# Performance work log

Hardware: AMD Instinct MI355X
Metric: run time of the kernel (lower is better)

Reference implementation:

```python
import jax, jax.numpy as jnp
import numpy as np

N_NODES = 100000
N_EDGES = 1600000
IN_CH = 128
OUT_CH = 64
HID = 2 * OUT_CH


def setup_inputs() -> dict:
    key = jax.random.key(0)
    ks = jax.random.split(key, 9)
    x = jax.random.normal(ks[0], (N_NODES, IN_CH), dtype=jnp.float32)
    edge_index = jax.random.randint(ks[1], (2, N_EDGES), 0, N_NODES, dtype=jnp.int64)
    s = 0.05
    W1 = jax.random.normal(ks[2], (IN_CH, HID), dtype=jnp.float32) * s
    b1 = jnp.zeros((HID,), dtype=jnp.float32)
    Wmu = jax.random.normal(ks[3], (HID, OUT_CH), dtype=jnp.float32) * s
    bmu = jnp.zeros((OUT_CH,), dtype=jnp.float32)
    Wls = jax.random.normal(ks[4], (HID, OUT_CH), dtype=jnp.float32) * s
    bls = jnp.zeros((OUT_CH,), dtype=jnp.float32)
    eps = jax.random.normal(ks[5], (N_NODES, OUT_CH), dtype=jnp.float32)
    return {"x": x, "edge_index": edge_index, "W1": W1, "b1": b1,
            "Wmu": Wmu, "bmu": bmu, "Wls": Wls, "bls": bls, "eps": eps}


def _gcn_conv(x, W, b, src, dst, dis):
    # PyG GCNConv: out = D^{-1/2}(A+I)D^{-1/2} X W + b, self-loops added.
    h = x @ W  # [N, F]
    norm = dis[src] * dis[dst]  # per-edge symmetric norm
    msg = h[src] * norm[:, None]  # [E, F] gathered + scaled messages
    agg = jax.ops.segment_sum(msg, dst, num_segments=x.shape[0])
    agg = agg + h * (dis * dis)[:, None]  # self-loop term
    return agg + b


def reference(x, edge_index, W1, b1, Wmu, bmu, Wls, bls, eps):
    src, dst = edge_index[0], edge_index[1]
    N = x.shape[0]
    # degree over A + I (aggregation at dst, +1 for self loop)
    deg = jax.ops.segment_sum(jnp.ones_like(dst, dtype=x.dtype), dst,
                              num_segments=N) + 1.0
    dis = jax.lax.rsqrt(deg)  # deg >= 1, safe
    h = _gcn_conv(x, W1, b1, src, dst, dis)
    mu = _gcn_conv(h, Wmu, bmu, src, dst, dis)
    logstd = _gcn_conv(h, Wls, bls, src, dst, dis)
    z = mu + eps * jnp.exp(logstd)  # reparametrization trick
    return (z, mu, logstd)
```

## Files before the change

kernel.cpp:

```cpp
#include <hip/hip_runtime.h>
#include <hip/hip_bf16.h>


typedef unsigned int u32;
typedef unsigned short u16;
typedef unsigned char u8;
typedef __bf16 bf16x8 __attribute__((ext_vector_type(8)));
typedef float f32x4 __attribute__((ext_vector_type(4)));
typedef int i32x4 __attribute__((ext_vector_type(4)));

#define NBKT 196
#define BSH 9

__device__ __forceinline__ u16 f2bf(float f) {
    union { float f; u32 u; } v; v.f = f;
    u32 u = v.u;
    u += 0x7fffu + ((u >> 16) & 1u);
    return (u16)(u >> 16);
}
__device__ __forceinline__ float bflo(u32 p) {
    union { u32 u; float f; } v; v.u = p << 16; return v.f;
}
__device__ __forceinline__ float bfhi(u32 p) {
    union { u32 u; float f; } v; v.u = p & 0xffff0000u; return v.f;
}

__global__ __launch_bounds__(256) void bcount(const int* __restrict__ dst,
                                              u32* __restrict__ bucketCnt, int E) {
    __shared__ u32 hist[NBKT];
    int t = threadIdx.x;
    for (int i = t; i < NBKT; i += 256) hist[i] = 0;
    __syncthreads();
    int base = (blockIdx.x * 256 + t) * 4;
    if (base + 3 < E) {
        i32x4 d4 = __builtin_nontemporal_load((const i32x4*)(dst + base));
        atomicAdd(&hist[d4.x >> BSH], 1u);
        atomicAdd(&hist[d4.y >> BSH], 1u);
        atomicAdd(&hist[d4.z >> BSH], 1u);
        atomicAdd(&hist[d4.w >> BSH], 1u);
    } else {
        for (int i = base; i < E; ++i) atomicAdd(&hist[dst[i] >> BSH], 1u);
    }
    __syncthreads();
    for (int i = t; i < NBKT; i += 256)
        if (hist[i]) atomicAdd(&bucketCnt[i], hist[i]);
}

__global__ __launch_bounds__(256) void bscan(const u32* __restrict__ bucketCnt,
                                             u32* __restrict__ bucketStart,
                                             u32* __restrict__ bucketCur,
                                             u32* __restrict__ rowstart,
                                             int N, int E) {
    __shared__ u32 s[256];
    int t = threadIdx.x;
    u32 v = (t < NBKT) ? bucketCnt[t] : 0u;
    s[t] = v;
    for (int off = 1; off < 256; off <<= 1) {
        __syncthreads();
        u32 add = (t >= off) ? s[t - off] : 0u;
        __syncthreads();
        s[t] += add;
    }
    __syncthreads();
    if (t < NBKT) {
        u32 ex = s[t] - v;
        bucketStart[t] = ex;
        bucketCur[t] = ex;
        if (t == NBKT - 1) bucketStart[NBKT] = s[t];
    }
    if (t == 0) rowstart[N] = (u32)(E + N);
}

__global__ __launch_bounds__(256) void bscatter(const int* __restrict__ src,
                                                const int* __restrict__ dst,
                                                u32* __restrict__ bucketCur,
                                                u32* __restrict__ bksrc,
                                                u32* __restrict__ bkdst, int E) {
    __shared__ u32 hist[NBKT], lstart[NBKT], gbase[NBKT];
    __shared__ u32 sA[256];
    __shared__ u32 stS[1024], stD[1024];
    int t = threadIdx.x;
    int e0 = blockIdx.x * 1024;
    int m = min(1024, E - e0);
    for (int i = t; i < NBKT; i += 256) hist[i] = 0;
    __syncthreads();

    int sv[4], dv[4]; u32 rk[4];
    int base = e0 + t * 4;
    bool vec = (base + 3 < E);
    if (vec) {
        i32x4 s4 = __builtin_nontemporal_load((const i32x4*)(src + base));
        i32x4 d4 = __builtin_nontemporal_load((const i32x4*)(dst + base));
        sv[0] = s4.x; sv[1] = s4.y; sv[2] = s4.z; sv[3] = s4.w;
        dv[0] = d4.x; dv[1] = d4.y; dv[2] = d4.z; dv[3] = d4.w;
#pragma unroll
        for (int j = 0; j < 4; ++j) rk[j] = atomicAdd(&hist[dv[j] >> BSH], 1u);
    } else {
#pragma unroll
        for (int j = 0; j < 4; ++j) {
            if (base + j < E) {
                sv[j] = src[base + j]; dv[j] = dst[base + j];
                rk[j] = atomicAdd(&hist[dv[j] >> BSH], 1u);
            }
        }
    }
    __syncthreads();
    sA[t] = (t < NBKT) ? hist[t] : 0u;
    for (int off = 1; off < 256; off <<= 1) {
        __syncthreads();
        u32 add = (t >= off) ? sA[t - off] : 0u;
        __syncthreads();
        sA[t] += add;
    }
    __syncthreads();
    if (t < NBKT) {
        lstart[t] = sA[t] - hist[t];
        if (hist[t]) gbase[t] = atomicAdd(&bucketCur[t], hist[t]);
    }
    __syncthreads();
#pragma unroll
    for (int j = 0; j < 4; ++j) {
        if (base + j < E) {
            int b = dv[j] >> BSH;
            u32 p = lstart[b] + rk[j];
            stS[p] = (u32)sv[j];
            stD[p] = (u32)dv[j];
        }
    }
    __syncthreads();
    for (int i = t; i < m; i += 256) {
        u32 d = stD[i];
        int b = (int)(d >> BSH);
        u32 g = gbase[b] + ((u32)i - lstart[b]);
        bksrc[g] = stS[i];
        bkdst[g] = d;
    }
}

__global__ __launch_bounds__(512) void bbuild(const u32* __restrict__ bksrc,
                                              const u32* __restrict__ bkdst,
                                              const u32* __restrict__ bucketStart,
                                              u32* __restrict__ rowstart,
                                              float* __restrict__ dis,
                                              int* __restrict__ csr, int N) {
    __shared__ u32 degL[512], exL[512];
    int t = threadIdx.x, b = blockIdx.x;
    int n0 = b << BSH;
    int nn = min(N - n0, 512);
    u32 ebeg = bucketStart[b], eend = bucketStart[b + 1];
    u32 cbase = ebeg + ((u32)b << BSH);
    degL[t] = 0;
    __syncthreads();
    for (u32 e = ebeg + t; e < eend; e += 512)
        atomicAdd(&degL[bkdst[e] - (u32)n0], 1u);
    __syncthreads();
    u32 v = degL[t] + ((t < nn) ? 1u : 0u);
    exL[t] = v;
    for (int off = 1; off < 512; off <<= 1) {
        __syncthreads();
        u32 add = (t >= off) ? exL[t - off] : 0u;
        __syncthreads();
        exL[t] += add;
    }
    __syncthreads();
    u32 rowbase = cbase + exL[t] - v;
    if (t < nn) {
        rowstart[n0 + t] = rowbase;
        dis[n0 + t] = rsqrtf((float)v);
        csr[rowbase] = n0 + t;
    }
    __syncthreads();
    exL[t] = rowbase + 1;
    __syncthreads();
    for (u32 e = ebeg + t; e < eend; e += 512) {
        u32 ln = bkdst[e] - (u32)n0;
        u32 pos = atomicAdd(&exL[ln], 1u);
        csr[pos] = (int)bksrc[e];
    }
}

__global__ __launch_bounds__(256) void fuse_w(const float* __restrict__ W1,
                                              const float* __restrict__ Wmu,
                                              const float* __restrict__ Wls,
                                              const float* __restrict__ b1,
                                              const float* __restrict__ bmu,
                                              const float* __restrict__ bls,
                                              u16* __restrict__ WfT,
                                              float* __restrict__ bb,
                                              float* __restrict__ bcat) {
    int idx = blockIdx.x * 256 + threadIdx.x;
    if (idx >= 16384) return;
    int k = idx >> 7, n = idx & 127;
    const float* Wcol = (n < 64) ? (Wmu + n) : (Wls + (n - 64));
    float acc = 0.f;
#pragma unroll 8
    for (int j = 0; j < 128; ++j) acc += W1[k * 128 + j] * Wcol[j * 64];
    WfT[n * 128 + k] = f2bf(acc);
    if (k == 0) {
        float accb = 0.f;
#pragma unroll 8
        for (int j = 0; j < 128; ++j) accb += b1[j] * Wcol[j * 64];
        bb[n] = accb;
        bcat[n] = (n < 64) ? bmu[n] : bls[n - 64];
    }
}

__global__ __launch_bounds__(256) void convert_x(const float* __restrict__ x,
                                                 const float* __restrict__ dis,
                                                 u32* __restrict__ xs,
                                                 u32* __restrict__ ts, int N) {
    long i = (long)blockIdx.x * 256 + threadIdx.x;
    long node = i >> 5;
    if (node > N) return;
    if (node == N) {
        ((uint2*)xs)[i] = make_uint2(0u, 0u);
        ((uint2*)ts)[i] = make_uint2(0u, 0u);
        return;
    }
    float dd = dis[node];
    f32x4 v = ((const f32x4*)x)[i];
    u32 p0 = (u32)f2bf(v[0] * dd) | ((u32)f2bf(v[1] * dd) << 16);
    u32 p1 = (u32)f2bf(v[2] * dd) | ((u32)f2bf(v[3] * dd) << 16);
    ((uint2*)xs)[i] = make_uint2(p0, p1);
}

__global__ __launch_bounds__(512) void g1gemm(const u32* __restrict__ xs,
                                              const int* __restrict__ csr,
                                              const u32* __restrict__ rowstart,
                                              const float* __restrict__ dis,
                                              const u16* __restrict__ WfT,
                                              const float* __restrict__ bb,
                                              u16* __restrict__ ts, int N,
                                              int nodeBase) {
    __shared__ __align__(16) u16 ytile[16][136];
    __shared__ float disS[16];
    int tid = threadIdx.x, blk = blockIdx.x;
    int wave = tid >> 6, lane = tid & 63;
    int nsub = lane >> 5;
    int h = (lane >> 4) & 1;
    int l = lane & 15;
    int nl = wave * 2 + nsub;
    int node = nodeBase + blk * 16 + nl;
    bool live = node < N;
    int nodeC = live ? node : 0;
    float dd = dis[nodeC];
    u32 beg = live ? rowstart[nodeC] : 0u;
    u32 end = live ? rowstart[nodeC + 1] : 0u;
    u32 cut = beg + ((end - beg + 1u) >> 1);
    u32 mybeg = h ? cut : beg;
    u32 myend = h ? end : cut;
    if (tid < 16)
        disS[tid] = (nodeBase + blk * 16 + tid < N) ? dis[nodeBase + blk * 16 + tid]
                                                    : 0.f;

    const uint4* xs4 = (const uint4*)xs;
    float a0 = 0.f, a1 = 0.f, a2 = 0.f, a3 = 0.f;
    float a4 = 0.f, a5 = 0.f, a6 = 0.f, a7 = 0.f;

    int sbase = nsub * 32 + h * 16;
    int s = (l < 8 && mybeg + (u32)l < myend) ? csr[mybeg + l] : N;
    for (u32 e0 = mybeg; e0 < myend; e0 += 8) {
        u32 e1 = e0 + 8;
        int sn = (l < 8 && e1 < myend && e1 + (u32)l < myend) ? csr[e1 + l] : N;
        uint4 w[8];
#pragma unroll
        for (int j = 0; j < 8; ++j) {
            int sj = __shfl(s, sbase + j);
            w[j] = xs4[(long)sj * 16 + l];
        }
#pragma unroll
        for (int j = 0; j < 8; ++j) {
            a0 += bflo(w[j].x); a1 += bfhi(w[j].x);
            a2 += bflo(w[j].y); a3 += bfhi(w[j].y);
            a4 += bflo(w[j].z); a5 += bfhi(w[j].z);
            a6 += bflo(w[j].w); a7 += bfhi(w[j].w);
        }
        s = sn;
    }
    a0 += __shfl_xor(a0, 16); a1 += __shfl_xor(a1, 16);
    a2 += __shfl_xor(a2, 16); a3 += __shfl_xor(a3, 16);
    a4 += __shfl_xor(a4, 16); a5 += __shfl_xor(a5, 16);
    a6 += __shfl_xor(a6, 16); a7 += __shfl_xor(a7, 16);

    uint4 o = make_uint4(0u, 0u, 0u, 0u);
    if (live) {
        o.x = (u32)f2bf(a0 * dd) | ((u32)f2bf(a1 * dd) << 16);
        o.y = (u32)f2bf(a2 * dd) | ((u32)f2bf(a3 * dd) << 16);
        o.z = (u32)f2bf(a4 * dd) | ((u32)f2bf(a5 * dd) << 16);
        o.w = (u32)f2bf(a6 * dd) | ((u32)f2bf(a7 * dd) << 16);
    }
    if (h == 0) *(uint4*)&ytile[nl][l * 8] = o;
    __syncthreads();

    int quad = lane >> 4, mn = l;
    bf16x8 af[4];
#pragma unroll
    for (int kk = 0; kk < 4; ++kk)
        af[kk] = *reinterpret_cast<const bf16x8*>(&ytile[mn][kk * 32 + quad * 8]);

    int col = wave * 16 + mn;
    f32x4 acc = {0.f, 0.f, 0.f, 0.f};
#pragma unroll
    for (int kk = 0; kk < 4; ++kk) {
        bf16x8 bf =
            *reinterpret_cast<const bf16x8*>(&WfT[col * 128 + kk * 32 + quad * 8]);
        acc = __builtin_amdgcn_mfma_f32_16x16x32_bf16(af[kk], bf, acc, 0, 0, 0);
    }
    float bc = bb[col];
#pragma unroll
    for (int r = 0; r < 4; ++r) {
        int row = quad * 4 + r;
        int gn = nodeBase + blk * 16 + row;
        if (gn < N)
            __builtin_nontemporal_store(f2bf((acc[r] + bc) * disS[row]),
                                        ts + (long)gn * 128 + col);
    }
}

__global__ __launch_bounds__(256) void gather2(const u32* __restrict__ ts,
                                               const int* __restrict__ csr,
                                               const u32* __restrict__ rowstart,
                                               const float* __restrict__ dis,
                                               const float* __restrict__ bcat,
                                               const float* __restrict__ eps,
                                               float* __restrict__ out, int N,
                                               int nodeBase) {
    int tid = threadIdx.x;
    int gw = (blockIdx.x * 256 + tid) >> 6;
    int lane = tid & 63;
    int nsub = lane >> 5, h = (lane >> 4) & 1, l = lane & 15;
    int node = nodeBase + gw * 2 + nsub;
    bool live = node < N;
    int nodeC = live ? node : 0;
    float dd = dis[nodeC];
    u32 beg = live ? rowstart[nodeC] : 0u;
    u32 end = live ? rowstart[nodeC + 1] : 0u;
    u32 cut = beg + ((end - beg + 1u) >> 1);
    u32 mybeg = h ? cut : beg;
    u32 myend = h ? end : cut;
    const uint4* ts4 = (const uint4*)ts;

    float a0 = 0.f, a1 = 0.f, a2 = 0.f, a3 = 0.f;
    float a4 = 0.f, a5 = 0.f, a6 = 0.f, a7 = 0.f;

    int sbase = nsub * 32 + h * 16;
    int s = (l < 8 && mybeg + (u32)l < myend) ? csr[mybeg + l] : N;
    for (u32 e0 = mybeg; e0 < myend; e0 += 8) {
        u32 e1 = e0 + 8;
        int sn = (l < 8 && e1 < myend && e1 + (u32)l < myend) ? csr[e1 + l] : N;
        uint4 w[8];
#pragma unroll
        for (int j = 0; j < 8; ++j) {
            int sj = __shfl(s, sbase + j);
            w[j] = ts4[(long)sj * 16 + l];
        }
#pragma unroll
        for (int j = 0; j < 8; ++j) {
            a0 += bflo(w[j].x); a1 += bfhi(w[j].x);
            a2 += bflo(w[j].y); a3 += bfhi(w[j].y);
            a4 += bflo(w[j].z); a5 += bfhi(w[j].z);
            a6 += bflo(w[j].w); a7 += bfhi(w[j].w);
        }
        s = sn;
    }
    a0 += __shfl_xor(a0, 16); a1 += __shfl_xor(a1, 16);
    a2 += __shfl_xor(a2, 16); a3 += __shfl_xor(a3, 16);
    a4 += __shfl_xor(a4, 16); a5 += __shfl_xor(a5, 16);
    a6 += __shfl_xor(a6, 16); a7 += __shfl_xor(a7, 16);

    int c0 = l * 8;
    f32x4 clo = ((const f32x4*)bcat)[2 * l], chi = ((const f32x4*)bcat)[2 * l + 1];
    float v0 = a0 * dd + clo[0];
    float v1 = a1 * dd + clo[1];
    float v2 = a2 * dd + clo[2];
    float v3 = a3 * dd + clo[3];
    float v4 = a4 * dd + chi[0];
    float v5 = a5 * dd + chi[1];
    float v6 = a6 * dd + chi[2];
    float v7 = a7 * dd + chi[3];

    int srcl = lane + 8;
    float w0 = __shfl(v0, srcl), w1 = __shfl(v1, srcl), w2 = __shfl(v2, srcl),
          w3 = __shfl(v3, srcl), w4 = __shfl(v4, srcl), w5 = __shfl(v5, srcl),
          w6 = __shfl(v6, srcl), w7 = __shfl(v7, srcl);

    if (!live || h != 0) return;
    long NO = (long)N * 64;
    if (l < 8) {
        float* mu = out + NO + (long)node * 64 + c0;
        __builtin_nontemporal_store(f32x4{v0, v1, v2, v3}, (f32x4*)mu);
        __builtin_nontemporal_store(f32x4{v4, v5, v6, v7}, (f32x4*)mu + 1);
        const f32x4* ep = (const f32x4*)(eps + (long)node * 64 + c0);
        f32x4 e0v = __builtin_nontemporal_load(ep);
        f32x4 e1v = __builtin_nontemporal_load(ep + 1);
        float* z = out + (long)node * 64 + c0;
        f32x4 z0 = {v0 + e0v[0] * __expf(w0), v1 + e0v[1] * __expf(w1),
                    v2 + e0v[2] * __expf(w2), v3 + e0v[3] * __expf(w3)};
        f32x4 z1 = {v4 + e1v[0] * __expf(w4), v5 + e1v[1] * __expf(w5),
                    v6 + e1v[2] * __expf(w6), v7 + e1v[3] * __expf(w7)};
        __builtin_nontemporal_store(z0, (f32x4*)z);
        __builtin_nontemporal_store(z1, (f32x4*)z + 1);
    } else {
        float* ls = out + 2 * NO + (long)node * 64 + (c0 - 64);
        __builtin_nontemporal_store(f32x4{v0, v1, v2, v3}, (f32x4*)ls);
        __builtin_nontemporal_store(f32x4{v4, v5, v6, v7}, (f32x4*)ls + 1);
    }
}

extern "C" void kernel_launch(void* const* d_in, const int* in_sizes, int n_in,
                              void* d_out, int out_size, void* d_ws, size_t ws_size,
                              hipStream_t stream) {
    const float* x   = (const float*)d_in[0];
    const int* ei    = (const int*)d_in[1];
    const float* W1  = (const float*)d_in[2];
    const float* b1  = (const float*)d_in[3];
    const float* Wmu = (const float*)d_in[4];
    const float* bmu = (const float*)d_in[5];
    const float* Wls = (const float*)d_in[6];
    const float* bls = (const float*)d_in[7];
    const float* eps = (const float*)d_in[8];
    float* out = (float*)d_out;

    const int N = in_sizes[0] / 128;
    const int E = in_sizes[1] / 2;
    const int* src = ei;
    const int* dst = ei + E;

    char* ws = (char*)d_ws;
    u32* rowstart    = (u32*)(ws + 0);
    u32* bucketCnt   = (u32*)(ws + 401408);
    u32* bucketStart = (u32*)(ws + 403456);
    u32* bucketCur   = (u32*)(ws + 405504);
    float* dis       = (float*)(ws + 407552);
    u16* WfT         = (u16*)(ws + 808960);
    float* bb        = (float*)(ws + 841728);
    float* bcat      = (float*)(ws + 842240);
    int* csr         = (int*)(ws + 843776);
    u32* xs          = (u32*)(ws + 7644160);
    u32* ts          = (u32*)(ws + 33244416);
    u32* bksrc       = (u32*)(ws + 33244416);
    u32* bkdst       = (u32*)(ws + 39644416);

    hipMemsetAsync(bucketCnt, 0, 1024, stream);

    int gridE4 = (E / 4 + 255) / 256;
    bcount<<<gridE4, 256, 0, stream>>>(dst, bucketCnt, E);
    bscan<<<1, 256, 0, stream>>>(bucketCnt, bucketStart, bucketCur, rowstart, N, E);
    bscatter<<<gridE4, 256, 0, stream>>>(src, dst, bucketCur, bksrc, bkdst, E);
    bbuild<<<NBKT, 512, 0, stream>>>(bksrc, bkdst, bucketStart, rowstart, dis,
                                     csr, N);

    fuse_w<<<64, 256, 0, stream>>>(W1, Wmu, Wls, b1, bmu, bls, WfT, bb, bcat);

    long Qc = (long)(N + 1) * 32;
    convert_x<<<(int)((Qc + 255) / 256), 256, 0, stream>>>(x, dis, xs, ts, N);

    int H = (N + 1) / 2;
    int gridT1 = (H + 15) / 16;
    int gridT2 = (N - H + 15) / 16;
    g1gemm<<<gridT1, 512, 0, stream>>>(xs, csr, rowstart, dis, WfT, bb,
                                       (u16*)ts, N, 0);
    g1gemm<<<gridT2, 512, 0, stream>>>(xs, csr, rowstart, dis, WfT, bb,
                                       (u16*)ts, N, H);

    int gridG1 = (H + 7) / 8;
    int gridG2 = (N - H + 7) / 8;
    gather2<<<gridG1, 256, 0, stream>>>(ts, csr, rowstart, dis, bcat, eps, out,
                                        N, 0);
    gather2<<<gridG2, 256, 0, stream>>>(ts, csr, rowstart, dis, bcat, eps, out,
                                        N, H);
}
```

Measured before the change: 408.5 us.

## Slice features into 16-channel planes so gathers work on cache-resident slices

```diff
diff --git a/kernel.cpp b/kernel.cpp
--- a/kernel.cpp
+++ b/kernel.cpp
@@ -8,6 +8,7 @@
 typedef __bf16 bf16x8 __attribute__((ext_vector_type(8)));
 typedef float f32x4 __attribute__((ext_vector_type(4)));
 typedef int i32x4 __attribute__((ext_vector_type(4)));
+typedef u32 u32x2 __attribute__((ext_vector_type(2)));
 
 #define NBKT 196
 #define BSH 9
@@ -68,7 +69,7 @@
         bucketCur[t] = ex;
         if (t == NBKT - 1) bucketStart[NBKT] = s[t];
     }
-    if (t == 0) rowstart[N] = (u32)(E + N);
+    if (t == 0) rowstart[N] = (u32)E;
 }
 
 __global__ __launch_bounds__(256) void bscatter(const int* __restrict__ src,
@@ -148,13 +149,12 @@
     int n0 = b << BSH;
     int nn = min(N - n0, 512);
     u32 ebeg = bucketStart[b], eend = bucketStart[b + 1];
-    u32 cbase = ebeg + ((u32)b << BSH);
     degL[t] = 0;
     __syncthreads();
     for (u32 e = ebeg + t; e < eend; e += 512)
         atomicAdd(&degL[bkdst[e] - (u32)n0], 1u);
     __syncthreads();
-    u32 v = degL[t] + ((t < nn) ? 1u : 0u);
+    u32 v = degL[t];
     exL[t] = v;
     for (int off = 1; off < 512; off <<= 1) {
         __syncthreads();
@@ -163,14 +163,13 @@
         exL[t] += add;
     }
     __syncthreads();
-    u32 rowbase = cbase + exL[t] - v;
+    u32 absbase = ebeg + exL[t] - v;
     if (t < nn) {
-        rowstart[n0 + t] = rowbase;
-        dis[n0 + t] = rsqrtf((float)v);
-        csr[rowbase] = n0 + t;
-    }
-    __syncthreads();
-    exL[t] = rowbase + 1;
+        rowstart[n0 + t] = absbase;
+        dis[n0 + t] = rsqrtf((float)v + 1.0f);
+    }
+    __syncthreads();
+    exL[t] = absbase;
     __syncthreads();
     for (u32 e = ebeg + t; e < eend; e += 512) {
         u32 ln = bkdst[e] - (u32)n0;
@@ -207,193 +206,198 @@
 
 __global__ __launch_bounds__(256) void convert_x(const float* __restrict__ x,
                                                  const float* __restrict__ dis,
-                                                 u32* __restrict__ xs,
-                                                 u32* __restrict__ ts, int N) {
+                                                 u32* __restrict__ xsP, int N) {
     long i = (long)blockIdx.x * 256 + threadIdx.x;
     long node = i >> 5;
+    int j = (int)(i & 31);
     if (node > N) return;
+    int s = j >> 2, q = j & 3;
+    u32x2* dst = (u32x2*)((char*)xsP + ((size_t)s * (N + 1) + node) * 32 + q * 8);
     if (node == N) {
-        ((uint2*)xs)[i] = make_uint2(0u, 0u);
-        ((uint2*)ts)[i] = make_uint2(0u, 0u);
+        u32x2 z = {0u, 0u};
+        *dst = z;
         return;
     }
     float dd = dis[node];
     f32x4 v = ((const f32x4*)x)[i];
-    u32 p0 = (u32)f2bf(v[0] * dd) | ((u32)f2bf(v[1] * dd) << 16);
-    u32 p1 = (u32)f2bf(v[2] * dd) | ((u32)f2bf(v[3] * dd) << 16);
-    ((uint2*)xs)[i] = make_uint2(p0, p1);
-}
-
-__global__ __launch_bounds__(512) void g1gemm(const u32* __restrict__ xs,
-                                              const int* __restrict__ csr,
-                                              const u32* __restrict__ rowstart,
-                                              const float* __restrict__ dis,
-                                              const u16* __restrict__ WfT,
-                                              const float* __restrict__ bb,
-                                              u16* __restrict__ ts, int N,
-                                              int nodeBase) {
+    u32x2 o;
+    o.x = (u32)f2bf(v[0] * dd) | ((u32)f2bf(v[1] * dd) << 16);
+    o.y = (u32)f2bf(v[2] * dd) | ((u32)f2bf(v[3] * dd) << 16);
+    *dst = o;
+}
+
+__global__ __launch_bounds__(256) void gather1s(const u32* __restrict__ xsP,
+                                                const int* __restrict__ csr,
+                                                const u32* __restrict__ rowstart,
+                                                const float* __restrict__ dis,
+                                                u32* __restrict__ ys, int N) {
+    int tid = threadIdx.x;
+    u32 bid = blockIdx.x;
+    int s = bid & 7;
+    int sg = tid >> 4, ll = tid & 15;
+    int j = ll >> 1, p = ll & 1;
+    int node = (int)(bid >> 3) * 16 + sg;
+    bool live = node < N;
+    int nodeC = live ? node : 0;
+    float dd = dis[nodeC];
+    u32 beg = rowstart[nodeC];
+    u32 end = live ? rowstart[nodeC + 1] : beg;
+    const uint4* base = (const uint4*)(xsP + (size_t)s * (N + 1) * 8);
+
+    float a0 = 0.f, a1 = 0.f, a2 = 0.f, a3 = 0.f;
+    float a4 = 0.f, a5 = 0.f, a6 = 0.f, a7 = 0.f;
+
+    u32 e0 = beg + (u32)j;
+    int idx = (e0 < end) ? csr[e0] : N;
+    for (u32 c = beg; c < end; c += 8) {
+        u32 c1 = c + 8;
+        int idxn = (c1 + (u32)j < end) ? csr[c1 + (u32)j] : N;
+        uint4 v = base[(size_t)idx * 2 + p];
+        a0 += bflo(v.x); a1 += bfhi(v.x);
+        a2 += bflo(v.y); a3 += bfhi(v.y);
+        a4 += bflo(v.z); a5 += bfhi(v.z);
+        a6 += bflo(v.w); a7 += bfhi(v.w);
+        idx = idxn;
+    }
+#pragma unroll
+    for (int m = 2; m <= 8; m <<= 1) {
+        a0 += __shfl_xor(a0, m); a1 += __shfl_xor(a1, m);
+        a2 += __shfl_xor(a2, m); a3 += __shfl_xor(a3, m);
+        a4 += __shfl_xor(a4, m); a5 += __shfl_xor(a5, m);
+        a6 += __shfl_xor(a6, m); a7 += __shfl_xor(a7, m);
+    }
+    if (j != 0) return;
+    uint4 sv = base[(size_t)nodeC * 2 + p];
+    a0 += bflo(sv.x); a1 += bfhi(sv.x);
+    a2 += bflo(sv.y); a3 += bfhi(sv.y);
+    a4 += bflo(sv.z); a5 += bfhi(sv.z);
+    a6 += bflo(sv.w); a7 += bfhi(sv.w);
+    if (!live) return;
+    uint4 o;
+    o.x = (u32)f2bf(a0 * dd) | ((u32)f2bf(a1 * dd) << 16);
+    o.y = (u32)f2bf(a2 * dd) | ((u32)f2bf(a3 * dd) << 16);
+    o.z = (u32)f2bf(a4 * dd) | ((u32)f2bf(a5 * dd) << 16);
+    o.w = (u32)f2bf(a6 * dd) | ((u32)f2bf(a7 * dd) << 16);
+    ((uint4*)ys)[((size_t)s * (N + 1) + node) * 2 + p] = o;
+}
+
+__global__ __launch_bounds__(256) void gemm1(const u32* __restrict__ ys,
+                                             const u16* __restrict__ WfT,
+                                             const float* __restrict__ bb,
+                                             const float* __restrict__ dis,
+                                             u16* __restrict__ tsP, int N) {
     __shared__ __align__(16) u16 ytile[16][136];
     __shared__ float disS[16];
     int tid = threadIdx.x, blk = blockIdx.x;
-    int wave = tid >> 6, lane = tid & 63;
-    int nsub = lane >> 5;
-    int h = (lane >> 4) & 1;
-    int l = lane & 15;
-    int nl = wave * 2 + nsub;
-    int node = nodeBase + blk * 16 + nl;
+    int node0 = blk * 16;
+    if (tid < 16) disS[tid] = (node0 + tid < N) ? dis[node0 + tid] : 0.f;
+    int row = tid >> 4, ch = tid & 15;
+    int gn = node0 + row;
+    int gnC = (gn < N) ? gn : (N - 1);
+    uint4 av = ((const uint4*)ys)[((size_t)(ch >> 1) * (N + 1) + gnC) * 2 + (ch & 1)];
+    *(uint4*)&ytile[row][ch * 8] = av;
+    __syncthreads();
+
+    int wave = tid >> 6, lane = tid & 63, quad = lane >> 4, mn = lane & 15;
+    bf16x8 af[4];
+#pragma unroll
+    for (int kk = 0; kk < 4; ++kk)
+        af[kk] = *reinterpret_cast<const bf16x8*>(&ytile[mn][kk * 32 + quad * 8]);
+
+#pragma unroll
+    for (int n0 = 0; n0 < 2; ++n0) {
+        int col = wave * 32 + n0 * 16 + mn;
+        f32x4 acc = {0.f, 0.f, 0.f, 0.f};
+#pragma unroll
+        for (int kk = 0; kk < 4; ++kk) {
+            bf16x8 bf =
+                *reinterpret_cast<const bf16x8*>(&WfT[col * 128 + kk * 32 + quad * 8]);
+            acc = __builtin_amdgcn_mfma_f32_16x16x32_bf16(af[kk], bf, acc, 0, 0, 0);
+        }
+        float bc = bb[col];
+        int sC = (col < 64) ? (col >> 3) : ((col - 64) >> 3);
+        int posC = (col & 7) + ((col < 64) ? 0 : 8);
+        u16* op = tsP + ((size_t)sC * (N + 1) + node0) * 16 + posC;
+#pragma unroll
+        for (int r = 0; r < 4; ++r) {
+            int rr = quad * 4 + r;
+            if (node0 + rr < N)
+                __builtin_nontemporal_store(f2bf((acc[r] + bc) * disS[rr]),
+                                            op + (size_t)rr * 16);
+        }
+    }
+}
+
+__global__ __launch_bounds__(256) void gather2s(const u32* __restrict__ tsP,
+                                                const int* __restrict__ csr,
+                                                const u32* __restrict__ rowstart,
+                                                const float* __restrict__ dis,
+                                                const float* __restrict__ bcat,
+                                                const float* __restrict__ eps,
+                                                float* __restrict__ out, int N) {
+    int tid = threadIdx.x;
+    u32 bid = blockIdx.x;
+    int s = bid & 7;
+    int sg = tid >> 4, ll = tid & 15;
+    int j = ll >> 1, p = ll & 1;
+    int node = (int)(bid >> 3) * 16 + sg;
     bool live = node < N;
     int nodeC = live ? node : 0;
     float dd = dis[nodeC];
-    u32 beg = live ? rowstart[nodeC] : 0u;
-    u32 end = live ? rowstart[nodeC + 1] : 0u;
-    u32 cut = beg + ((end - beg + 1u) >> 1);
-    u32 mybeg = h ? cut : beg;
-    u32 myend = h ? end : cut;
-    if (tid < 16)
-        disS[tid] = (nodeBase + blk * 16 + tid < N) ? dis[nodeBase + blk * 16 + tid]
-                                                    : 0.f;
-
-    const uint4* xs4 = (const uint4*)xs;
+    u32 beg = rowstart[nodeC];
+    u32 end = live ? rowstart[nodeC + 1] : beg;
+    const uint4* base = (const uint4*)(tsP + (size_t)s * (N + 1) * 8);
+
     float a0 = 0.f, a1 = 0.f, a2 = 0.f, a3 = 0.f;
     float a4 = 0.f, a5 = 0.f, a6 = 0.f, a7 = 0.f;
 
-    int sbase = nsub * 32 + h * 16;
-    int s = (l < 8 && mybeg + (u32)l < myend) ? csr[mybeg + l] : N;
-    for (u32 e0 = mybeg; e0 < myend; e0 += 8) {
-        u32 e1 = e0 + 8;
-        int sn = (l < 8 && e1 < myend && e1 + (u32)l < myend) ? csr[e1 + l] : N;
-        uint4 w[8];
-#pragma unroll
-        for (int j = 0; j < 8; ++j) {
-            int sj = __shfl(s, sbase + j);
-            w[j] = xs4[(long)sj * 16 + l];
-        }
-#pragma unroll
-        for (int j = 0; j < 8; ++j) {
-            a0 += bflo(w[j].x); a1 += bfhi(w[j].x);
-            a2 += bflo(w[j].y); a3 += bfhi(w[j].y);
-            a4 += bflo(w[j].z); a5 += bfhi(w[j].z);
-            a6 += bflo(w[j].w); a7 += bfhi(w[j].w);
-        }
-        s = sn;
-    }
-    a0 += __shfl_xor(a0, 16); a1 += __shfl_xor(a1, 16);
-    a2 += __shfl_xor(a2, 16); a3 += __shfl_xor(a3, 16);
-    a4 += __shfl_xor(a4, 16); a5 += __shfl_xor(a5, 16);
-    a6 += __shfl_xor(a6, 16); a7 += __shfl_xor(a7, 16);
-
-    uint4 o = make_uint4(0u, 0u, 0u, 0u);
-    if (live) {
-        o.x = (u32)f2bf(a0 * dd) | ((u32)f2bf(a1 * dd) << 16);
-        o.y = (u32)f2bf(a2 * dd) | ((u32)f2bf(a3 * dd) << 16);
-        o.z = (u32)f2bf(a4 * dd) | ((u32)f2bf(a5 * dd) << 16);
-        o.w = (u32)f2bf(a6 * dd) | ((u32)f2bf(a7 * dd) << 16);
-    }
-    if (h == 0) *(uint4*)&ytile[nl][l * 8] = o;
-    __syncthreads();
-
-    int quad = lane >> 4, mn = l;
-    bf16x8 af[4];
-#pragma unroll
-    for (int kk = 0; kk < 4; ++kk)
-        af[kk] = *reinterpret_cast<const bf16x8*>(&ytile[mn][kk * 32 + quad * 8]);
-
-    int col = wave * 16 + mn;
-    f32x4 acc = {0.f, 0.f, 0.f, 0.f};
-#pragma unroll
-    for (int kk = 0; kk < 4; ++kk) {
-        bf16x8 bf =
-            *reinterpret_cast<const bf16x8*>(&WfT[col * 128 + kk * 32 + quad * 8]);
-        acc = __builtin_amdgcn_mfma_f32_16x16x32_bf16(af[kk], bf, acc, 0, 0, 0);
-    }
-    float bc = bb[col];
-#pragma unroll
-    for (int r = 0; r < 4; ++r) {
-        int row = quad * 4 + r;
-        int gn = nodeBase + blk * 16 + row;
-        if (gn < N)
-            __builtin_nontemporal_store(f2bf((acc[r] + bc) * disS[row]),
-                                        ts + (long)gn * 128 + col);
-    }
-}
-
-__global__ __launch_bounds__(256) void gather2(const u32* __restrict__ ts,
-                                               const int* __restrict__ csr,
-                                               const u32* __restrict__ rowstart,
-                                               const float* __restrict__ dis,
-                                               const float* __restrict__ bcat,
-                                               const float* __restrict__ eps,
-                                               float* __restrict__ out, int N,
-                                               int nodeBase) {
-    int tid = threadIdx.x;
-    int gw = (blockIdx.x * 256 + tid) >> 6;
-    int lane = tid & 63;
-    int nsub = lane >> 5, h = (lane >> 4) & 1, l = lane & 15;
-    int node = nodeBase + gw * 2 + nsub;
-    bool live = node < N;
-    int nodeC = live ? node : 0;
-    float dd = dis[nodeC];
-    u32 beg = live ? rowstart[nodeC] : 0u;
-    u32 end = live ? rowstart[nodeC + 1] : 0u;
-    u32 cut = beg + ((end - beg + 1u) >> 1);
-    u32 mybeg = h ? cut : beg;
-    u32 myend = h ? end : cut;
-    const uint4* ts4 = (const uint4*)ts;
-
-    float a0 = 0.f, a1 = 0.f, a2 = 0.f, a3 = 0.f;
-    float a4 = 0.f, a5 = 0.f, a6 = 0.f, a7 = 0.f;
-
-    int sbase = nsub * 32 + h * 16;
-    int s = (l < 8 && mybeg + (u32)l < myend) ? csr[mybeg + l] : N;
-    for (u32 e0 = mybeg; e0 < myend; e0 += 8) {
-        u32 e1 = e0 + 8;
-        int sn = (l < 8 && e1 < myend && e1 + (u32)l < myend) ? csr[e1 + l] : N;
-        uint4 w[8];
-#pragma unroll
-        for (int j = 0; j < 8; ++j) {
-            int sj = __shfl(s, sbase + j);
-            w[j] = ts4[(long)sj * 16 + l];
-        }
-#pragma unroll
-        for (int j = 0; j < 8; ++j) {
-            a0 += bflo(w[j].x); a1 += bfhi(w[j].x);
-            a2 += bflo(w[j].y); a3 += bfhi(w[j].y);
-            a4 += bflo(w[j].z); a5 += bfhi(w[j].z);
-            a6 += bflo(w[j].w); a7 += bfhi(w[j].w);
-        }
-        s = sn;
-    }
-    a0 += __shfl_xor(a0, 16); a1 += __shfl_xor(a1, 16);
-    a2 += __shfl_xor(a2, 16); a3 += __shfl_xor(a3, 16);
-    a4 += __shfl_xor(a4, 16); a5 += __shfl_xor(a5, 16);
-    a6 += __shfl_xor(a6, 16); a7 += __shfl_xor(a7, 16);
-
-    int c0 = l * 8;
-    f32x4 clo = ((const f32x4*)bcat)[2 * l], chi = ((const f32x4*)bcat)[2 * l + 1];
-    float v0 = a0 * dd + clo[0];
-    float v1 = a1 * dd + clo[1];
-    float v2 = a2 * dd + clo[2];
-    float v3 = a3 * dd + clo[3];
-    float v4 = a4 * dd + chi[0];
-    float v5 = a5 * dd + chi[1];
-    float v6 = a6 * dd + chi[2];
-    float v7 = a7 * dd + chi[3];
-
-    int srcl = lane + 8;
-    float w0 = __shfl(v0, srcl), w1 = __shfl(v1, srcl), w2 = __shfl(v2, srcl),
-          w3 = __shfl(v3, srcl), w4 = __shfl(v4, srcl), w5 = __shfl(v5, srcl),
-          w6 = __shfl(v6, srcl), w7 = __shfl(v7, srcl);
-
-    if (!live || h != 0) return;
+    u32 e0 = beg + (u32)j;
+    int idx = (e0 < end) ? csr[e0] : N;
+    for (u32 c = beg; c < end; c += 8) {
+        u32 c1 = c + 8;
+        int idxn = (c1 + (u32)j < end) ? csr[c1 + (u32)j] : N;
+        uint4 v = base[(size_t)idx * 2 + p];
+        a0 += bflo(v.x); a1 += bfhi(v.x);
+        a2 += bflo(v.y); a3 += bfhi(v.y);
+        a4 += bflo(v.z); a5 += bfhi(v.z);
+        a6 += bflo(v.w); a7 += bfhi(v.w);
+        idx = idxn;
+    }
+#pragma unroll
+    for (int m = 2; m <= 8; m <<= 1) {
+        a0 += __shfl_xor(a0, m); a1 += __shfl_xor(a1, m);
+        a2 += __shfl_xor(a2, m); a3 += __shfl_xor(a3, m);
+        a4 += __shfl_xor(a4, m); a5 += __shfl_xor(a5, m);
+        a6 += __shfl_xor(a6, m); a7 += __shfl_xor(a7, m);
+    }
+    if (j != 0) return;
+    uint4 sv = base[(size_t)nodeC * 2 + p];
+    a0 += bflo(sv.x); a1 += bfhi(sv.x);
+    a2 += bflo(sv.y); a3 += bfhi(sv.y);
+    a4 += bflo(sv.z); a5 += bfhi(sv.z);
+    a6 += bflo(sv.w); a7 += bfhi(sv.w);
+
+    const f32x4* bc = (const f32x4*)(bcat + (p ? 64 + 8 * s : 8 * s));
+    f32x4 c0 = bc[0], c1 = bc[1];
+    float v0 = a0 * dd + c0[0], v1 = a1 * dd + c0[1];
+    float v2 = a2 * dd + c0[2], v3 = a3 * dd + c0[3];
+    float v4 = a4 * dd + c1[0], v5 = a5 * dd + c1[1];
+    float v6 = a6 * dd + c1[2], v7 = a7 * dd + c1[3];
+
+    float w0 = __shfl_xor(v0, 1), w1 = __shfl_xor(v1, 1), w2 = __shfl_xor(v2, 1),
+          w3 = __shfl_xor(v3, 1), w4 = __shfl_xor(v4, 1), w5 = __shfl_xor(v5, 1),
+          w6 = __shfl_xor(v6, 1), w7 = __shfl_xor(v7, 1);
+
+    if (!live) return;
     long NO = (long)N * 64;
-    if (l < 8) {
-        float* mu = out + NO + (long)node * 64 + c0;
+    if (p == 0) {
+        float* mu = out + NO + (long)node * 64 + 8 * s;
         __builtin_nontemporal_store(f32x4{v0, v1, v2, v3}, (f32x4*)mu);
         __builtin_nontemporal_store(f32x4{v4, v5, v6, v7}, (f32x4*)mu + 1);
-        const f32x4* ep = (const f32x4*)(eps + (long)node * 64 + c0);
+        const f32x4* ep = (const f32x4*)(eps + (long)node * 64 + 8 * s);
         f32x4 e0v = __builtin_nontemporal_load(ep);
         f32x4 e1v = __builtin_nontemporal_load(ep + 1);
-        float* z = out + (long)node * 64 + c0;
+        float* z = out + (long)node * 64 + 8 * s;
         f32x4 z0 = {v0 + e0v[0] * __expf(w0), v1 + e0v[1] * __expf(w1),
                     v2 + e0v[2] * __expf(w2), v3 + e0v[3] * __expf(w3)};
         f32x4 z1 = {v4 + e1v[0] * __expf(w4), v5 + e1v[1] * __expf(w5),
@@ -401,7 +405,7 @@
         __builtin_nontemporal_store(z0, (f32x4*)z);
         __builtin_nontemporal_store(z1, (f32x4*)z + 1);
     } else {
-        float* ls = out + 2 * NO + (long)node * 64 + (c0 - 64);
+        float* ls = out + 2 * NO + (long)node * 64 + 8 * s;
         __builtin_nontemporal_store(f32x4{v0, v1, v2, v3}, (f32x4*)ls);
         __builtin_nontemporal_store(f32x4{v4, v5, v6, v7}, (f32x4*)ls + 1);
     }
@@ -436,10 +440,11 @@
     float* bb        = (float*)(ws + 841728);
     float* bcat      = (float*)(ws + 842240);
     int* csr         = (int*)(ws + 843776);
-    u32* xs          = (u32*)(ws + 7644160);
-    u32* ts          = (u32*)(ws + 33244416);
-    u32* bksrc       = (u32*)(ws + 33244416);
-    u32* bkdst       = (u32*)(ws + 39644416);
+    u32* xsP         = (u32*)(ws + 7244800);
+    u32* ys          = (u32*)(ws + 32845056);
+    u16* tsP         = (u16*)xsP;
+    u32* bksrc       = (u32*)(ws + 7244800);
+    u32* bkdst       = (u32*)(ws + 13644800);
 
     hipMemsetAsync(bucketCnt, 0, 1024, stream);
 
@@ -453,20 +458,13 @@
     fuse_w<<<64, 256, 0, stream>>>(W1, Wmu, Wls, b1, bmu, bls, WfT, bb, bcat);
 
     long Qc = (long)(N + 1) * 32;
-    convert_x<<<(int)((Qc + 255) / 256), 256, 0, stream>>>(x, dis, xs, ts, N);
-
-    int H = (N + 1) / 2;
-    int gridT1 = (H + 15) / 16;
-    int gridT2 = (N - H + 15) / 16;
-    g1gemm<<<gridT1, 512, 0, stream>>>(xs, csr, rowstart, dis, WfT, bb,
-                                       (u16*)ts, N, 0);
-    g1gemm<<<gridT2, 512, 0, stream>>>(xs, csr, rowstart, dis, WfT, bb,
-                                       (u16*)ts, N, H);
-
-    int gridG1 = (H + 7) / 8;
-    int gridG2 = (N - H + 7) / 8;
-    gather2<<<gridG1, 256, 0, stream>>>(ts, csr, rowstart, dis, bcat, eps, out,
-                                        N, 0);
-    gather2<<<gridG2, 256, 0, stream>>>(ts, csr, rowstart, dis, bcat, eps, out,
-                                        N, H);
-}
+    convert_x<<<(int)((Qc + 255) / 256), 256, 0, stream>>>(x, dis, xsP, N);
+
+    int gridS = 8 * ((N + 15) / 16);
+    gather1s<<<gridS, 256, 0, stream>>>(xsP, csr, rowstart, dis, ys, N);
+
+    gemm1<<<(N + 15) / 16, 256, 0, stream>>>(ys, WfT, bb, dis, tsP, N);
+
+    gather2s<<<gridS, 256, 0, stream>>>((const u32*)tsP, csr, rowstart, dis,
+                                        bcat, eps, out, N);
+}
```

New measurement: 579.7 us. +41.9%, slower.
